# Kernel optimization log

Hardware: AMD Instinct MI355X
Metric: run time of the kernel (lower is better)

The kernel has to match this reference:

```python
import jax, jax.numpy as jnp
import numpy as np

B, S, D = 4, 2048, 768
H = 12
HD = D // H  # 64


def setup_inputs() -> dict:
    key = jax.random.key(0)
    k1, k2, k3 = jax.random.split(key, 3)
    x = jax.random.normal(k1, (B, S, D), dtype=jnp.float32)
    w_qkv = jax.random.normal(k2, (D, 3 * D), dtype=jnp.float32) * (1.0 / np.sqrt(D))
    b_qkv = jnp.zeros((3 * D,), dtype=jnp.float32)
    w_proj = jax.random.normal(k3, (D, D), dtype=jnp.float32) * (1.0 / np.sqrt(D))
    b_proj = jnp.zeros((D,), dtype=jnp.float32)
    return {"x": x, "w_qkv": w_qkv, "b_qkv": b_qkv, "w_proj": w_proj, "b_proj": b_proj}


def reference(x, w_qkv, b_qkv, w_proj, b_proj):
    b, s, d = x.shape
    qkv = x @ w_qkv + b_qkv                      # [B,S,3D]
    q, k, v = jnp.split(qkv, 3, axis=-1)
    # [B,S,D] -> [B,H,S,HD]
    q = q.reshape(b, s, H, HD).transpose(0, 2, 1, 3)
    k = k.reshape(b, s, H, HD).transpose(0, 2, 1, 3)
    v = v.reshape(b, s, H, HD).transpose(0, 2, 1, 3)
    scores = jnp.einsum("bhqd,bhkd->bhqk", q, k) / jnp.sqrt(jnp.float32(HD))
    causal = jnp.tril(jnp.ones((s, s), dtype=bool))
    scores = jnp.where(causal[None, None, :, :], scores, jnp.float32(-jnp.inf))
    attn = jax.nn.softmax(scores, axis=-1)       # dropout p=0.0 -> identity
    out = jnp.einsum("bhqk,bhkd->bhqd", attn, v)  # [B,H,S,HD]
    out = out.transpose(0, 2, 1, 3).reshape(b, s, d)
    return out @ w_proj + b_proj
```

## Files before the change

### kernel.cpp

```cpp
#include <hip/hip_runtime.h>
#include <hip/hip_bf16.h>

typedef __hip_bfloat16 bf16;
typedef __bf16 bf16x8 __attribute__((ext_vector_type(8)));
typedef float f32x4 __attribute__((ext_vector_type(4)));
typedef unsigned int uint32x2 __attribute__((ext_vector_type(2)));

#define MFMA(a, b, c) __builtin_amdgcn_mfma_f32_16x16x32_bf16(a, b, c, 0, 0, 0)
#define EXP2F(x) __builtin_exp2f(x)

constexpr int Bn = 4, Sn = 2048, Dn = 768, Hn = 12;
constexpr int N3 = 3 * Dn;
constexpr int Mrows = Bn * Sn;

constexpr size_t XB_OFF    = 0;
constexpr size_t WQKV_OFF  = 12582912;
constexpr size_t WPROJ_OFF = 16121856;
constexpr size_t Q_OFF     = 17301504;
constexpr size_t K_OFF     = 29884416;
constexpr size_t VT_OFF    = 42467328;
constexpr size_t O_OFF     = 55050240;

#define QSCALE 0.1803368801111243f

__device__ __forceinline__ void gload16(const void* g, void* l) {
  __builtin_amdgcn_global_load_lds((__attribute__((address_space(1))) void*)g,
                                   (__attribute__((address_space(3))) void*)l,
                                   16, 0, 0);
}

__device__ __forceinline__ unsigned int cvt_pk_bf16(float lo, float hi) {
  unsigned int r;
  asm("v_cvt_pk_bf16_f32 %0, %1, %2" : "=v"(r) : "v"(lo), "v"(hi));
  return r;
}

__global__ __launch_bounds__(256) void cvt_x_kernel(const float* __restrict__ in,
                                                    bf16* __restrict__ out, int n4) {
  int i = blockIdx.x * 256 + threadIdx.x;
  if (i >= n4) return;
  float4 f = reinterpret_cast<const float4*>(in)[i];
  uint2 o;
  o.x = cvt_pk_bf16(f.x, f.y);
  o.y = cvt_pk_bf16(f.z, f.w);
  reinterpret_cast<uint2*>(out)[i] = o;
}

__global__ __launch_bounds__(256) void transpose_cvt2(const float* __restrict__ inA,
                                                      bf16* __restrict__ outA,
                                                      const float* __restrict__ inB,
                                                      bf16* __restrict__ outB) {
  __shared__ float tile[32][33];
  const int bx = blockIdx.x;
  const float* in;
  bf16* out;
  int N, n0;
  if (bx < 72) { in = inA; out = outA; N = N3; n0 = bx * 32; }
  else         { in = inB; out = outB; N = Dn; n0 = (bx - 72) * 32; }
  const int k0 = blockIdx.y * 32;
  const int tx = threadIdx.x & 31, ty = threadIdx.x >> 5;
  for (int r = ty; r < 32; r += 8)
    tile[r][tx] = in[(size_t)(k0 + r) * N + n0 + tx];
  __syncthreads();
  for (int r = ty; r < 32; r += 8)
    out[(size_t)(n0 + r) * Dn + k0 + tx] = __float2bfloat16(tile[tx][r]);
}

__global__ __launch_bounds__(256) void gemm_qkv(const bf16* __restrict__ A,
                                                const bf16* __restrict__ BT,
                                                const float* __restrict__ bias,
                                                bf16* __restrict__ Qo,
                                                bf16* __restrict__ Ko,
                                                bf16* __restrict__ Vt) {
  __shared__ __align__(16) bf16 As[2][128 * 32];
  __shared__ __align__(16) bf16 Bs[2][128 * 32];
  const int tid = threadIdx.x;
  const int m0 = blockIdx.x * 128, n0 = blockIdx.y * 128;
  const int w = tid >> 6, lane = tid & 63;
  const int wr = w >> 1, wc = w & 1;
  const int lr = lane & 15, lg = lane >> 4;

  f32x4 acc[4][4] = {};

  auto stage = [&](int k0, int sb) {
    for (int r = 0; r < 2; ++r) {
      int c = tid + r * 256;
      int row = c >> 2, ch = c & 3;
      int gch = ch ^ ((row >> 1) & 3);
      gload16(A + (size_t)(m0 + row) * Dn + k0 + gch * 8, &As[sb][c * 8]);
      gload16(BT + (size_t)(n0 + row) * Dn + k0 + gch * 8, &Bs[sb][c * 8]);
    }
  };

  stage(0, 0);
  __syncthreads();

  const int sw = (lr >> 1) & 3;
  const int aoff = (wr * 64 + lr) * 32 + ((lg ^ sw) << 3);
  const int boff = (wc * 64 + lr) * 32 + ((lg ^ sw) << 3);
  int buf = 0;

  for (int kt = 0; kt < 24; ++kt) {
    if (kt < 23) stage((kt + 1) * 32, buf ^ 1);
    bf16x8 af[4], bfr[4];
    for (int mi = 0; mi < 4; ++mi)
      af[mi] = *reinterpret_cast<const bf16x8*>(&As[buf][aoff + mi * 512]);
    for (int ni = 0; ni < 4; ++ni)
      bfr[ni] = *reinterpret_cast<const bf16x8*>(&Bs[buf][boff + ni * 512]);
    for (int mi = 0; mi < 4; ++mi)
      for (int ni = 0; ni < 4; ++ni)
        acc[mi][ni] = MFMA(af[mi], bfr[ni], acc[mi][ni]);
    __syncthreads();
    buf ^= 1;
  }

  for (int ni = 0; ni < 4; ++ni) {
    const int col = n0 + wc * 64 + ni * 16 + lr;
    const float bv = bias[col];
    const int seg = (col >= Dn) + (col >= 2 * Dn);
    const int d = col - seg * Dn;
    const int h = d >> 6, hd = d & 63;
    for (int mi = 0; mi < 4; ++mi) {
      f32x4 v = acc[mi][ni];
      const int row0 = m0 + wr * 64 + mi * 16 + lg * 4;
      const int b = row0 >> 11, s0 = row0 & 2047;
      const size_t bh = (size_t)(b * Hn + h);
      if (seg == 2) {
        uint2 pk;
        pk.x = cvt_pk_bf16(v[0] + bv, v[1] + bv);
        pk.y = cvt_pk_bf16(v[2] + bv, v[3] + bv);
        *reinterpret_cast<uint2*>(&Vt[(bh * 64 + hd) * Sn + s0]) = pk;
      } else if (seg == 0) {
        for (int r = 0; r < 4; ++r)
          Qo[(bh * Sn + s0 + r) * 64 + hd] = __float2bfloat16((v[r] + bv) * QSCALE);
      } else {
        for (int r = 0; r < 4; ++r)
          Ko[(bh * Sn + s0 + r) * 64 + hd] = __float2bfloat16(v[r] + bv);
      }
    }
  }
}

__global__ __launch_bounds__(256) void attn_fwd(const bf16* __restrict__ Q,
                                                const bf16* __restrict__ K,
                                                const bf16* __restrict__ Vt,
                                                bf16* __restrict__ O) {
  __shared__ __align__(16) bf16 Ks[2][64 * 64];
  __shared__ __align__(16) bf16 Vs[2][64 * 64];
  const int tid = threadIdx.x, w = tid >> 6, lane = tid & 63;
  const int lr = lane & 15, lg = lane >> 4;
  const int bid = blockIdx.x;
  const int qt = 31 - (bid / 48);
  const int bh = bid % 48;
  const int q0 = qt * 64;
  const size_t base = (size_t)bh * Sn * 64;
  const int wrow = q0 + w * 16;

  bf16x8 qf[2];
  for (int kk = 0; kk < 2; ++kk)
    qf[kk] = *reinterpret_cast<const bf16x8*>(
        Q + base + (size_t)(wrow + lr) * 64 + kk * 32 + lg * 8);

  f32x4 o[4] = {};
  f32x4 lacc = {};

  const int nt = qt + 1;

  const int c0 = tid, c1 = tid + 256;
  const int r0 = c0 >> 3, s0w = (c0 & 7) ^ (r0 & 7);
  const int r1 = c1 >> 3, s1w = (c1 & 7) ^ (r1 & 7);
  const bf16* kp0 = K + base + r0 * 64 + s0w * 8;
  const bf16* kp1 = K + base + r1 * 64 + s1w * 8;
  const bf16* vp0 = Vt + base + (size_t)r0 * Sn + s0w * 8;
  const bf16* vp1 = Vt + base + (size_t)r1 * Sn + s1w * 8;

  gload16(kp0, &Ks[0][c0 * 8]);
  gload16(kp1, &Ks[0][c1 * 8]);
  gload16(vp0, &Vs[0][c0 * 8]);
  gload16(vp1, &Vs[0][c1 * 8]);
  kp0 += 4096; kp1 += 4096; vp0 += 64; vp1 += 64;
  __syncthreads();

  int buf = 0;
  for (int t = 0; t < nt; ++t) {
    if (t + 1 < nt) {
      const int sb = buf ^ 1;
      gload16(kp0, &Ks[sb][c0 * 8]);
      gload16(kp1, &Ks[sb][c1 * 8]);
      gload16(vp0, &Vs[sb][c0 * 8]);
      gload16(vp1, &Vs[sb][c1 * 8]);
      kp0 += 4096; kp1 += 4096; vp0 += 64; vp1 += 64;
    }

    f32x4 sf[4];
    __builtin_amdgcn_s_setprio(1);
    for (int ni = 0; ni < 4; ++ni) {
      const int krow = ni * 16 + lr;
      bf16x8 kf0 = *reinterpret_cast<const bf16x8*>(&Ks[buf][krow * 64 + (lg ^ (lr & 7)) * 8]);
      bf16x8 kf1 = *reinterpret_cast<const bf16x8*>(&Ks[buf][krow * 64 + ((4 + lg) ^ (lr & 7)) * 8]);
      f32x4 z = {};
      z = MFMA(kf0, qf[0], z);
      z = MFMA(kf1, qf[1], z);
      sf[ni] = z;
    }
    __builtin_amdgcn_s_setprio(0);
    if (t == nt - 1) {
      const int qg = wrow + lr;
      for (int ni = 0; ni < 4; ++ni)
        for (int r = 0; r < 4; ++r) {
          int kg = t * 64 + ni * 16 + lg * 4 + r;
          if (kg > qg) sf[ni][r] = -1e30f;
        }
    }
    for (int ni = 0; ni < 4; ++ni) {
      f32x4 z = sf[ni];
      z[0] = EXP2F(z[0]);
      z[1] = EXP2F(z[1]);
      z[2] = EXP2F(z[2]);
      z[3] = EXP2F(z[3]);
      sf[ni] = z;
      lacc += z;
    }
    unsigned int Wv[4][2];
    for (int ni = 0; ni < 4; ++ni) {
      Wv[ni][0] = cvt_pk_bf16(sf[ni][0], sf[ni][1]);
      Wv[ni][1] = cvt_pk_bf16(sf[ni][2], sf[ni][3]);
    }
    __align__(16) unsigned int pw[2][4];
    for (int kk = 0; kk < 2; ++kk) {
      for (int h = 0; h < 2; ++h) {
        uint32x2 s32 = __builtin_amdgcn_permlane32_swap(Wv[2 * kk][h], Wv[2 * kk + 1][h],
                                                        false, false);
        uint32x2 s16 = __builtin_amdgcn_permlane16_swap(s32[0], s32[1], false, false);
        pw[kk][h]     = s16[0];
        pw[kk][2 + h] = s16[1];
      }
    }
    __builtin_amdgcn_s_setprio(1);
    for (int kk = 0; kk < 2; ++kk) {
      bf16x8 pf = *reinterpret_cast<const bf16x8*>(&pw[kk][0]);
      const int psw = ((kk * 4 + lg) ^ (lr & 7)) << 3;
      for (int di = 0; di < 4; ++di) {
        bf16x8 vf = *reinterpret_cast<const bf16x8*>(&Vs[buf][(di * 16 + lr) * 64 + psw]);
        o[di] = MFMA(vf, pf, o[di]);
      }
    }
    __builtin_amdgcn_s_setprio(0);
    __syncthreads();
    buf ^= 1;
  }

  float l = (lacc[0] + lacc[1]) + (lacc[2] + lacc[3]);
  l += __shfl_xor(l, 16);
  l += __shfl_xor(l, 32);
  const float inv = 1.0f / l;
  const int b = bh / Hn, h = bh % Hn;
  const size_t rowbase = ((size_t)b * Sn + wrow + lr) * Dn + h * 64;
  for (int di = 0; di < 4; ++di) {
    f32x4 ov = o[di];
    uint2 pk;
    pk.x = cvt_pk_bf16(ov[0] * inv, ov[1] * inv);
    pk.y = cvt_pk_bf16(ov[2] * inv, ov[3] * inv);
    *reinterpret_cast<uint2*>(&O[rowbase + di * 16 + lg * 4]) = pk;
  }
}

__global__ __launch_bounds__(256) void gemm_proj(const bf16* __restrict__ A,
                                                 const bf16* __restrict__ BT,
                                                 const float* __restrict__ bias,
                                                 float* __restrict__ out) {
  __shared__ __align__(16) bf16 As[2][128 * 32];
  __shared__ __align__(16) bf16 Bs[2][128 * 32];
  const int tid = threadIdx.x;
  const int m0 = blockIdx.x * 128, n0 = blockIdx.y * 128;
  const int w = tid >> 6, lane = tid & 63;
  const int wr = w >> 1, wc = w & 1;
  const int lr = lane & 15, lg = lane >> 4;

  f32x4 acc[4][4] = {};

  auto stage = [&](int k0, int sb) {
    for (int r = 0; r < 2; ++r) {
      int c = tid + r * 256;
      int row = c >> 2, ch = c & 3;
      int gch = ch ^ ((row >> 1) & 3);
      gload16(A + (size_t)(m0 + row) * Dn + k0 + gch * 8, &As[sb][c * 8]);
      gload16(BT + (size_t)(n0 + row) * Dn + k0 + gch * 8, &Bs[sb][c * 8]);
    }
  };

  stage(0, 0);
  __syncthreads();

  const int sw = (lr >> 1) & 3;
  const int aoff = (wr * 64 + lr) * 32 + ((lg ^ sw) << 3);
  const int boff = (wc * 64 + lr) * 32 + ((lg ^ sw) << 3);
  int buf = 0;

  for (int kt = 0; kt < 24; ++kt) {
    if (kt < 23) stage((kt + 1) * 32, buf ^ 1);
    bf16x8 af[4], bfr[4];
    for (int mi = 0; mi < 4; ++mi)
      af[mi] = *reinterpret_cast<const bf16x8*>(&As[buf][aoff + mi * 512]);
    for (int ni = 0; ni < 4; ++ni)
      bfr[ni] = *reinterpret_cast<const bf16x8*>(&Bs[buf][boff + ni * 512]);
    for (int mi = 0; mi < 4; ++mi)
      for (int ni = 0; ni < 4; ++ni)
        acc[mi][ni] = MFMA(af[mi], bfr[ni], acc[mi][ni]);
    __syncthreads();
    buf ^= 1;
  }

  for (int ni = 0; ni < 4; ++ni) {
    const int col = n0 + wc * 64 + ni * 16 + lr;
    const float bv = bias[col];
    for (int mi = 0; mi < 4; ++mi) {
      f32x4 v = acc[mi][ni];
      for (int r = 0; r < 4; ++r) {
        const int row = m0 + wr * 64 + mi * 16 + lg * 4 + r;
        out[(size_t)row * Dn + col] = v[r] + bv;
      }
    }
  }
}

extern "C" void kernel_launch(void* const* d_in, const int* in_sizes, int n_in,
                              void* d_out, int out_size, void* d_ws, size_t ws_size,
                              hipStream_t stream) {
  const float* x      = (const float*)d_in[0];
  const float* w_qkv  = (const float*)d_in[1];
  const float* b_qkv  = (const float*)d_in[2];
  const float* w_proj = (const float*)d_in[3];
  const float* b_proj = (const float*)d_in[4];
  float* out = (float*)d_out;

  char* ws = (char*)d_ws;
  bf16* xb     = (bf16*)(ws + XB_OFF);
  bf16* wqkvT  = (bf16*)(ws + WQKV_OFF);
  bf16* wprojT = (bf16*)(ws + WPROJ_OFF);
  bf16* Qb     = (bf16*)(ws + Q_OFF);
  bf16* Kb     = (bf16*)(ws + K_OFF);
  bf16* Vtb    = (bf16*)(ws + VT_OFF);
  bf16* Ob     = (bf16*)(ws + O_OFF);

  cvt_x_kernel<<<(Mrows * Dn / 4 + 255) / 256, 256, 0, stream>>>(x, xb, Mrows * Dn / 4);
  transpose_cvt2<<<dim3(96, Dn / 32), 256, 0, stream>>>(w_qkv, wqkvT, w_proj, wprojT);
  gemm_qkv<<<dim3(Mrows / 128, N3 / 128), 256, 0, stream>>>(xb, wqkvT, b_qkv, Qb, Kb, Vtb);
  attn_fwd<<<32 * 48, 256, 0, stream>>>(Qb, Kb, Vtb, Ob);
  gemm_proj<<<dim3(Mrows / 128, Dn / 128), 256, 0, stream>>>(Ob, wprojT, b_proj, out);
}
```

Baseline: 137.3 us.

## Triple-buffer GEMM LDS staging with explicit vmcnt waits and single barrier

Both the QKV and projection GEMMs move from double- to triple-buffered LDS staging. Loads run two k-tiles ahead, and each iteration waits with an explicit s_waitcnt vmcnt(4) plus one s_barrier instead of two __syncthreads. This is meant to hide global-to-LDS load latency and cut barrier stalls, at the cost of more LDS per block (which may lower occupancy). Correctness depends on the vmcnt count matching the four async loads issued per stage.

```diff
diff --git a/kernel.cpp b/kernel.cpp
--- a/kernel.cpp
+++ b/kernel.cpp
@@ -72,8 +72,8 @@
                                                 bf16* __restrict__ Qo,
                                                 bf16* __restrict__ Ko,
                                                 bf16* __restrict__ Vt) {
-  __shared__ __align__(16) bf16 As[2][128 * 32];
-  __shared__ __align__(16) bf16 Bs[2][128 * 32];
+  __shared__ __align__(16) bf16 As[3][128 * 32];
+  __shared__ __align__(16) bf16 Bs[3][128 * 32];
   const int tid = threadIdx.x;
   const int m0 = blockIdx.x * 128, n0 = blockIdx.y * 128;
   const int w = tid >> 6, lane = tid & 63;
@@ -93,25 +93,32 @@
   };
 
   stage(0, 0);
-  __syncthreads();
+  stage(32, 1);
 
   const int sw = (lr >> 1) & 3;
   const int aoff = (wr * 64 + lr) * 32 + ((lg ^ sw) << 3);
   const int boff = (wc * 64 + lr) * 32 + ((lg ^ sw) << 3);
-  int buf = 0;
+  int bufi = 0;
 
   for (int kt = 0; kt < 24; ++kt) {
-    if (kt < 23) stage((kt + 1) * 32, buf ^ 1);
+    if (kt + 1 < 24) {
+      asm volatile("s_waitcnt vmcnt(4)" ::: "memory");
+    } else {
+      asm volatile("s_waitcnt vmcnt(0)" ::: "memory");
+    }
+    __builtin_amdgcn_sched_barrier(0);
+    __builtin_amdgcn_s_barrier();
+    __builtin_amdgcn_sched_barrier(0);
+    if (kt + 2 < 24) stage((kt + 2) * 32, (bufi + 2) % 3);
     bf16x8 af[4], bfr[4];
     for (int mi = 0; mi < 4; ++mi)
-      af[mi] = *reinterpret_cast<const bf16x8*>(&As[buf][aoff + mi * 512]);
+      af[mi] = *reinterpret_cast<const bf16x8*>(&As[bufi][aoff + mi * 512]);
     for (int ni = 0; ni < 4; ++ni)
-      bfr[ni] = *reinterpret_cast<const bf16x8*>(&Bs[buf][boff + ni * 512]);
+      bfr[ni] = *reinterpret_cast<const bf16x8*>(&Bs[bufi][boff + ni * 512]);
     for (int mi = 0; mi < 4; ++mi)
       for (int ni = 0; ni < 4; ++ni)
         acc[mi][ni] = MFMA(af[mi], bfr[ni], acc[mi][ni]);
-    __syncthreads();
-    buf ^= 1;
+    bufi = (bufi + 1) % 3;
   }
 
   for (int ni = 0; ni < 4; ++ni) {
@@ -269,8 +276,8 @@
                                                  const bf16* __restrict__ BT,
                                                  const float* __restrict__ bias,
                                                  float* __restrict__ out) {
-  __shared__ __align__(16) bf16 As[2][128 * 32];
-  __shared__ __align__(16) bf16 Bs[2][128 * 32];
+  __shared__ __align__(16) bf16 As[3][128 * 32];
+  __shared__ __align__(16) bf16 Bs[3][128 * 32];
   const int tid = threadIdx.x;
   const int m0 = blockIdx.x * 128, n0 = blockIdx.y * 128;
   const int w = tid >> 6, lane = tid & 63;
@@ -290,25 +297,32 @@
   };
 
   stage(0, 0);
-  __syncthreads();
+  stage(32, 1);
 
   const int sw = (lr >> 1) & 3;
   const int aoff = (wr * 64 + lr) * 32 + ((lg ^ sw) << 3);
   const int boff = (wc * 64 + lr) * 32 + ((lg ^ sw) << 3);
-  int buf = 0;
+  int bufi = 0;
 
   for (int kt = 0; kt < 24; ++kt) {
-    if (kt < 23) stage((kt + 1) * 32, buf ^ 1);
+    if (kt + 1 < 24) {
+      asm volatile("s_waitcnt vmcnt(4)" ::: "memory");
+    } else {
+      asm volatile("s_waitcnt vmcnt(0)" ::: "memory");
+    }
+    __builtin_amdgcn_sched_barrier(0);
+    __builtin_amdgcn_s_barrier();
+    __builtin_amdgcn_sched_barrier(0);
+    if (kt + 2 < 24) stage((kt + 2) * 32, (bufi + 2) % 3);
     bf16x8 af[4], bfr[4];
     for (int mi = 0; mi < 4; ++mi)
-      af[mi] = *reinterpret_cast<const bf16x8*>(&As[buf][aoff + mi * 512]);
+      af[mi] = *reinterpret_cast<const bf16x8*>(&As[bufi][aoff + mi * 512]);
     for (int ni = 0; ni < 4; ++ni)
-      bfr[ni] = *reinterpret_cast<const bf16x8*>(&Bs[buf][boff + ni * 512]);
+      bfr[ni] = *reinterpret_cast<const bf16x8*>(&Bs[bufi][boff + ni * 512]);
     for (int mi = 0; mi < 4; ++mi)
       for (int ni = 0; ni < 4; ++ni)
         acc[mi][ni] = MFMA(af[mi], bfr[ni], acc[mi][ni]);
-    __syncthreads();
-    buf ^= 1;
+    bufi = (bufi + 1) % 3;
   }
 
   for (int ni = 0; ni < 4; ++ni) {
```

New measurement: 134.6 us (median of 2 runs). 2.0% less time.
